# Performance work log

Hardware: AMD Instinct MI355X
Metric: run time of the kernel (lower is better)

## Reference

```python
import jax, jax.numpy as jnp
import numpy as np

L = 8          # curve control points per chunk (self.l)
TS = 256       # curve spatial resolution (self.ts)


def setup_inputs() -> dict:
    key = jax.random.key(0)
    k1, k2 = jax.random.split(key)
    # full-resolution input image, values in [0,1)
    x = jax.random.uniform(k1, (4, 3, 1024, 1024), dtype=jnp.float32)
    # predicted curve parameters: 9*L = 72 channels at TS x TS
    param = jax.random.normal(k2, (4, 72, TS, TS), dtype=jnp.float32)
    return {"x": x, "param": param}


def _grid_sample_3d(vol, gx, gy, gz):
    """F.grid_sample(vol, grid, 'bilinear', 'border', align_corners=True)
    vol: [B,C,D,Hc,Wc]; gx,gy,gz: [B,H,W] normalized coords in [-1,1].
    Returns [B,H,W,C] (channels last)."""
    B, C, D, Hc, Wc = vol.shape
    # align_corners=True unnormalization + border padding (clamp coords)
    ix = jnp.clip((gx + 1.0) * 0.5 * (Wc - 1), 0.0, Wc - 1)
    iy = jnp.clip((gy + 1.0) * 0.5 * (Hc - 1), 0.0, Hc - 1)
    iz = jnp.clip((gz + 1.0) * 0.5 * (D - 1), 0.0, D - 1)
    x0f, y0f, z0f = jnp.floor(ix), jnp.floor(iy), jnp.floor(iz)
    wx, wy, wz = ix - x0f, iy - y0f, iz - z0f
    x0 = x0f.astype(jnp.int32); x1 = jnp.minimum(x0 + 1, Wc - 1)
    y0 = y0f.astype(jnp.int32); y1 = jnp.minimum(y0 + 1, Hc - 1)
    z0 = z0f.astype(jnp.int32); z1 = jnp.minimum(z0 + 1, D - 1)
    vol_t = vol.transpose(0, 2, 3, 4, 1)  # [B,D,Hc,Wc,C]
    b = jnp.arange(B)[:, None, None]      # [B,1,1]
    out = jnp.zeros(gx.shape + (C,), dtype=vol.dtype)
    for zi, wz_ in ((z0, 1.0 - wz), (z1, wz)):
        for yi, wy_ in ((y0, 1.0 - wy), (y1, wy)):
            for xi, wx_ in ((x0, 1.0 - wx), (x1, wx)):
                w = (wz_ * wy_ * wx_)[..., None]          # [B,H,W,1]
                out = out + w * vol_t[b, zi, yi, xi]      # gather -> [B,H,W,C]
    return out


def reference(x, param):
    # eval-mode forward of Generator.mapping + tanh (param precomputed by CNN)
    B, _, H, W = x.shape
    Hc, Wc = param.shape[-2], param.shape[-1]
    # torch.stack(torch.chunk(param,3,dim=1),dim=1) == reshape [B,3,3L,Hc,Wc]
    curve = param.reshape(B, 3, 3 * L, Hc, Wc)
    coordh = jnp.linspace(-1.0, 1.0, H, dtype=x.dtype)[:, None]  # varies over H
    coordw = jnp.linspace(-1.0, 1.0, W, dtype=x.dtype)[None, :]  # varies over W
    gx = jnp.broadcast_to(coordw, (B, H, W))
    gy = jnp.broadcast_to(coordh, (B, H, W))
    out = jnp.zeros((B, H, W, 3), dtype=x.dtype)
    for i in range(3):  # three curve chunks, z-coordinate = i-th color channel
        curve_i = curve[:, :, i * L:(i + 1) * L]          # [B,3,L,Hc,Wc]
        out = out + _grid_sample_3d(curve_i, gx, gy, x[:, i])
    return jnp.tanh(out.transpose(0, 3, 1, 2))            # [B,3,H,W]
```

## Files before the change

### kernel.cpp

```cpp
#include <hip/hip_runtime.h>
#include <math.h>

#define IMG 1024
#define HW (IMG * IMG)
#define TS 256
#define CH_STRIDE (TS * TS)
#define PARAM_B_STRIDE (72 * CH_STRIDE)
#define S_CONST (255.0f / 1023.0f)

#define ROWS 6
#define CELLS 34
#define CHS 45
#define CELL_DW 73
#define ROW_DW (CELLS * CELL_DW)
#define LDS_DW (ROWS * ROW_DW)
#define RUNS (ROWS * CHS)

__global__ __launch_bounds__(1024, 8) void curve3d_fused(
    const float* __restrict__ x, const float* __restrict__ param,
    float* __restrict__ out)
{
    __shared__ float sh[LDS_DW];
    int blk = blockIdx.x;
    blk = (blk & 7) * 256 + (blk >> 3);
    int wt = blk & 7;
    int ht = (blk >> 3) & 63;
    int b  = blk >> 9;
    int tid = threadIdx.x;

    int w0 = wt * 128, h0 = ht * 16;
    int xb = (int)((float)w0 * S_CONST);
    int yb = (int)((float)h0 * S_CONST);

    int wx = tid & 15;
    int wyl = (tid >> 4) & 3;
    int pxp = (tid >> 6) & 7;
    int pyp = tid >> 9;
    int tw = pxp * 16 + wx;
    int th = pyp * 4 + wyl;
    int w = w0 + tw;
    int ha = h0 + th;

    const float* xp = x + (size_t)b * 3 * HW + (size_t)ha * IMG + w;
    float xv[2][3];
#pragma unroll
    for (int i = 0; i < 3; ++i) {
        xv[0][i] = __builtin_nontemporal_load(xp + (size_t)i * HW);
        xv[1][i] = __builtin_nontemporal_load(xp + (size_t)i * HW + 8 * IMG);
    }

    const float* pb = param + (size_t)b * PARAM_B_STRIDE;
    {
        int off = tid & 31;
        int cgrp = tid >> 5;
        int c1 = 32 + cgrp;
        int cho0 = (cgrp / 5) * 8 + cgrp % 5 + 3;
        int cho1 = (c1 / 5) * 8 + c1 % 5 + 3;
        int vo0 = cho0 * CH_STRIDE + xb + off;
        int vo1 = cho1 * CH_STRIDE + xb + off;
        int lo0 = off * CELL_DW + (cho0 - 3);
        int lo1 = off * CELL_DW + (cho1 - 3);
        bool q1 = (cgrp < 13);
#pragma unroll
        for (int row = 0; row < ROWS; ++row) {
            int ys = min(yb + row, 255);
            const float* rb = pb + ys * TS;
            sh[row * ROW_DW + lo0] = rb[vo0];
            if (q1) sh[row * ROW_DW + lo1] = rb[vo1];
        }
    }
    if (tid < 2 * RUNS) {
        int run = tid >> 1;
        int xx = 32 + (tid & 1);
        unsigned row = (unsigned)run / (unsigned)CHS;
        int chc = run - (int)row * CHS;
        int cho = (chc / 5) * 8 + chc % 5 + 3;
        int ys = min(yb + (int)row, 255);
        int xs = min(xb + xx, 255);
        sh[(int)row * ROW_DW + xx * CELL_DW + (cho - 3)] =
            pb[(size_t)cho * CH_STRIDE + ys * TS + xs];
    }

    int zo[2][3]; float wz[2][3];
#pragma unroll
    for (int p = 0; p < 2; ++p)
#pragma unroll
        for (int i = 0; i < 3; ++i) {
            float f = fminf(fmaxf(fmaf(xv[p][i], 3.5f, 3.5f), 0.0f), 7.0f);
            int z = min((int)f, 6);
            zo[p][i] = z - 3;
            wz[p][i] = f - (float)z;
        }

    float ixf = (float)w * S_CONST; int x0 = (int)ixf; float wxf = ixf - (float)x0;
    int cb0 = (x0 - xb) * CELL_DW;
    int cb1 = (min(x0 + 1, 255) - xb) * CELL_DW;
    float u0 = 1.0f - wxf;

    float wcs[2][4]; int bofs[2][4];
#pragma unroll
    for (int p = 0; p < 2; ++p) {
        int h = ha + p * 8;
        float iyf = (float)h * S_CONST; int y0 = (int)iyf; float wyf = iyf - (float)y0;
        int rb0 = (y0 - yb) * ROW_DW;
        int rb1 = (min(y0 + 1, 255) - yb) * ROW_DW;
        float v0 = 1.0f - wyf;
        wcs[p][0] = v0 * u0;  wcs[p][1] = v0 * wxf;
        wcs[p][2] = wyf * u0; wcs[p][3] = wyf * wxf;
        bofs[p][0] = rb0 + cb0; bofs[p][1] = rb0 + cb1;
        bofs[p][2] = rb1 + cb0; bofs[p][3] = rb1 + cb1;
    }

    __syncthreads();

    float acc[2][3] = {{0.0f, 0.0f, 0.0f}, {0.0f, 0.0f, 0.0f}};
#pragma unroll
    for (int i = 0; i < 3; ++i) {
#pragma unroll
        for (int k = 0; k < 4; ++k) {
#pragma unroll
            for (int p = 0; p < 2; ++p) {
                const float* bp = sh + bofs[p][k] + zo[p][i];
                float wk = wcs[p][k];
                float wzi = wz[p][i];
#pragma unroll
                for (int c = 0; c < 3; ++c) {
                    float2 v;
                    __builtin_memcpy(&v, bp + (c * 3 + i) * 8, 8);
                    float t = fmaf(wzi, v.y - v.x, v.x);
                    acc[p][c] = fmaf(wk, t, acc[p][c]);
                }
            }
        }
    }

    float* op = out + (size_t)b * 3 * HW + (size_t)ha * IMG + w;
#pragma unroll
    for (int p = 0; p < 2; ++p) {
        float* opp = op + (size_t)(p * 8) * IMG;
#pragma unroll
        for (int c = 0; c < 3; ++c) {
            float e = __expf(2.0f * acc[p][c]);
            opp[(size_t)c * HW] = 1.0f - 2.0f / (e + 1.0f);
        }
    }
}

extern "C" void kernel_launch(void* const* d_in, const int* in_sizes, int n_in,
                              void* d_out, int out_size, void* d_ws, size_t ws_size,
                              hipStream_t stream) {
    const float* x = (const float*)d_in[0];
    const float* param = (const float*)d_in[1];
    float* out = (float*)d_out;
    curve3d_fused<<<dim3(4 * 64 * 8), dim3(1024), 0, stream>>>(x, param, out);
}
```

Measured before the change: 180.2 us.

## Interleave z-pairs per cell in LDS so three channel taps load contiguously

```diff
diff --git a/kernel.cpp b/kernel.cpp
--- a/kernel.cpp
+++ b/kernel.cpp
@@ -11,7 +11,7 @@
 #define ROWS 6
 #define CELLS 34
 #define CHS 45
-#define CELL_DW 73
+#define CELL_DW 78
 #define ROW_DW (CELLS * CELL_DW)
 #define LDS_DW (ROWS * ROW_DW)
 #define RUNS (ROWS * CHS)
@@ -53,20 +53,36 @@
     {
         int off = tid & 31;
         int cgrp = tid >> 5;
-        int c1 = 32 + cgrp;
-        int cho0 = (cgrp / 5) * 8 + cgrp % 5 + 3;
-        int cho1 = (c1 / 5) * 8 + c1 % 5 + 3;
-        int vo0 = cho0 * CH_STRIDE + xb + off;
-        int vo1 = cho1 * CH_STRIDE + xb + off;
-        int lo0 = off * CELL_DW + (cho0 - 3);
-        int lo1 = off * CELL_DW + (cho1 - 3);
+        int g0 = cgrp / 5, zp0 = cgrp % 5;
+        int c0_ = g0 / 3, i0_ = g0 % 3;
+        int vo0 = (g0 * 8 + zp0 + 3) * CH_STRIDE + xb + off;
+        int cb_ = off * CELL_DW;
+        int bA0 = cb_ + i0_ * 24 + c0_ * 2;
+        int lA0 = bA0 + zp0 * 6;
+        int lB0 = bA0 + (zp0 - 1) * 6 + 1;
+        bool a0 = (zp0 <= 3), b0 = (zp0 >= 1);
+        int cc1 = 32 + cgrp;
+        int g1 = cc1 / 5, zp1 = cc1 % 5;
+        int c1_ = g1 / 3, i1_ = g1 % 3;
+        int vo1 = (g1 * 8 + zp1 + 3) * CH_STRIDE + xb + off;
+        int bA1 = cb_ + i1_ * 24 + c1_ * 2;
+        int lA1 = bA1 + zp1 * 6;
+        int lB1 = bA1 + (zp1 - 1) * 6 + 1;
+        bool a1 = (zp1 <= 3), b1 = (zp1 >= 1);
         bool q1 = (cgrp < 13);
 #pragma unroll
         for (int row = 0; row < ROWS; ++row) {
             int ys = min(yb + row, 255);
             const float* rb = pb + ys * TS;
-            sh[row * ROW_DW + lo0] = rb[vo0];
-            if (q1) sh[row * ROW_DW + lo1] = rb[vo1];
+            int rofs = row * ROW_DW;
+            float v0 = rb[vo0];
+            if (a0) sh[rofs + lA0] = v0;
+            if (b0) sh[rofs + lB0] = v0;
+            if (q1) {
+                float v1 = rb[vo1];
+                if (a1) sh[rofs + lA1] = v1;
+                if (b1) sh[rofs + lB1] = v1;
+            }
         }
     }
     if (tid < 2 * RUNS) {
@@ -74,11 +90,14 @@
         int xx = 32 + (tid & 1);
         unsigned row = (unsigned)run / (unsigned)CHS;
         int chc = run - (int)row * CHS;
-        int cho = (chc / 5) * 8 + chc % 5 + 3;
+        int g = chc / 5, zp = chc % 5;
+        int ci = g / 3, ii = g % 3;
         int ys = min(yb + (int)row, 255);
         int xs = min(xb + xx, 255);
-        sh[(int)row * ROW_DW + xx * CELL_DW + (cho - 3)] =
-            pb[(size_t)cho * CH_STRIDE + ys * TS + xs];
+        float v = pb[(size_t)(g * 8 + zp + 3) * CH_STRIDE + ys * TS + xs];
+        int basz = (int)row * ROW_DW + xx * CELL_DW + ii * 24 + ci * 2;
+        if (zp <= 3) sh[basz + zp * 6] = v;
+        if (zp >= 1) sh[basz + (zp - 1) * 6 + 1] = v;
     }
 
     int zo[2][3]; float wz[2][3];
@@ -115,21 +134,22 @@
 
     float acc[2][3] = {{0.0f, 0.0f, 0.0f}, {0.0f, 0.0f, 0.0f}};
 #pragma unroll
-    for (int i = 0; i < 3; ++i) {
+    for (int p = 0; p < 2; ++p) {
 #pragma unroll
-        for (int k = 0; k < 4; ++k) {
+        for (int i = 0; i < 3; ++i) {
+            int zoff = i * 24 + 6 * zo[p][i];
+            float wzi = wz[p][i];
 #pragma unroll
-            for (int p = 0; p < 2; ++p) {
-                const float* bp = sh + bofs[p][k] + zo[p][i];
+            for (int k = 0; k < 4; ++k) {
+                const float2* q2 =
+                    reinterpret_cast<const float2*>(sh + bofs[p][k] + zoff);
+                float2 A = q2[0];
+                float2 B = q2[1];
+                float2 C = q2[2];
                 float wk = wcs[p][k];
-                float wzi = wz[p][i];
-#pragma unroll
-                for (int c = 0; c < 3; ++c) {
-                    float2 v;
-                    __builtin_memcpy(&v, bp + (c * 3 + i) * 8, 8);
-                    float t = fmaf(wzi, v.y - v.x, v.x);
-                    acc[p][c] = fmaf(wk, t, acc[p][c]);
-                }
+                acc[p][0] = fmaf(wk, fmaf(wzi, A.y - A.x, A.x), acc[p][0]);
+                acc[p][1] = fmaf(wk, fmaf(wzi, B.y - B.x, B.x), acc[p][1]);
+                acc[p][2] = fmaf(wk, fmaf(wzi, C.y - C.x, C.x), acc[p][2]);
             }
         }
     }
```

After: 186.5 us. 3.5% more time.
